# Performance work log

Hardware: AMD Instinct MI355X
Metric: run time of the kernel (lower is better)

## Reference

```python
import jax, jax.numpy as jnp
import numpy as np

D_H = 1024

def _binary_operator(e_i, e_j):
    a_i, kv_i = e_i
    a_j, kv_j = e_j
    return (a_j * a_i, a_j * kv_i + kv_j)

def setup_inputs() -> dict:
    key = jax.random.key(0)
    k1, k2 = jax.random.split(key)
    B, S, D = 4, 4096, 1024
    x = jax.random.normal(k1, (B, S, D), dtype=jnp.float32)
    # nn.Dense default lecun_normal-ish scale; plain scaled normal is fine for a reference
    W = jax.random.normal(k2, (D, 3 * D_H), dtype=jnp.float32) * (1.0 / np.sqrt(D))
    b = jnp.zeros((3 * D_H,), dtype=jnp.float32)
    return {"x": x, "W": W, "b": b}

def reference(x, W, b):
    # projection: (B,S,D) @ (D, 3*d_h)
    proj = jnp.einsum('bsd,dh->bsh', x, W) + b
    inp = jnp.tanh(proj[:, :, :D_H])                 # (B,S,d_h)
    gates = jax.nn.sigmoid(proj[:, :, D_H:])         # (B,S,2*d_h)
    input_gate, output_gate = jnp.split(gates, 2, axis=-1)
    forget_gate = 1.0 - input_gate                   # tied gates
    _, hidden = jax.lax.associative_scan(
        _binary_operator, (forget_gate, inp * input_gate), axis=1)
    return jnp.tanh(hidden) * output_gate            # (B,S,d_h)
```

## Files before the change

### kernel.cpp

```cpp
#include <hip/hip_runtime.h>
#include <hip/hip_bf16.h>
#include <cmath>

typedef _Float16 half8 __attribute__((ext_vector_type(8)));
typedef _Float16 half4 __attribute__((ext_vector_type(4)));
typedef float f32x4 __attribute__((ext_vector_type(4)));

#define M_DIM 16384
#define K_DIM 1024
#define N_DIM 3072
#define S_LEN 4096
#define NCHUNK 64
#define CLEN 64

#define OT_STRIDE 136

__device__ __forceinline__ float fast_sigmoid(float x) {
    return __builtin_amdgcn_rcpf(1.0f + __expf(-x));
}
__device__ __forceinline__ float fast_tanh(float x) {
    float t = __expf(-2.0f * __builtin_fabsf(x));
    float y = (1.0f - t) * __builtin_amdgcn_rcpf(1.0f + t);
    return __builtin_copysignf(y, x);
}

__global__ void k_cast_x(const float* __restrict__ x, _Float16* __restrict__ xb) {
    int i = blockIdx.x * blockDim.x + threadIdx.x;
    float4 v = reinterpret_cast<const float4*>(x)[i];
    half4 h;
    h.x = (_Float16)v.x; h.y = (_Float16)v.y;
    h.z = (_Float16)v.z; h.w = (_Float16)v.w;
    reinterpret_cast<half4*>(xb)[i] = h;
}

__global__ void k_cast_w(const float* __restrict__ W, _Float16* __restrict__ Wt) {
    __shared__ float t[64][65];
    const int k0 = (blockIdx.x / 48) * 64;
    const int n0 = (blockIdx.x % 48) * 64;
    const int c  = threadIdx.x & 63;
    const int r0 = threadIdx.x >> 6;
    #pragma unroll
    for (int i = 0; i < 16; ++i) {
        int r = r0 + i * 4;
        t[r][c] = W[(size_t)(k0 + r) * N_DIM + n0 + c];
    }
    __syncthreads();
    #pragma unroll
    for (int i = 0; i < 16; ++i) {
        int r = r0 + i * 4;
        Wt[(size_t)(n0 + r) * K_DIM + k0 + c] = (_Float16)t[c][r];
    }
}

__global__ __launch_bounds__(256, 3) void k_gemm(
    const _Float16* __restrict__ A,
    const _Float16* __restrict__ Bt,
    const float* __restrict__ bias,
    _Float16* __restrict__ G)
{
    __shared__ _Float16 lds[128 * OT_STRIDE];

    const int tid  = threadIdx.x;
    const int lane = tid & 63;
    const int w    = tid >> 6;
    const int wr   = w >> 1;
    const int wc   = w & 1;

    const int bid   = blockIdx.x;
    const int wg    = (bid & 7) * 384 + (bid >> 3);
    const int tileM = (wg / 24) * 128;
    const int tileN = (wg % 24) * 128;

    const int l3   = lane >> 3;
    const int c8   = lane & 7;
    const int scol = ((c8 ^ l3) << 3);
    const _Float16* gA = A  + (size_t)(tileM + w * 32 + l3) * K_DIM + scol;
    const _Float16* gB = Bt + (size_t)(tileN + w * 32 + l3) * K_DIM + scol;
    _Float16* const sA = lds + w * 2048;
    _Float16* const sB = lds + 8192 + w * 2048;

    const int l15 = lane & 15;
    const int hi  = lane >> 4;
    const int swz = (l15 & 7) << 3;
    const int o0  = (hi * 8)      ^ swz;
    const int o1  = (32 + hi * 8) ^ swz;
    const _Float16* arow = lds + (wr * 64 + l15) * 64;
    const _Float16* brow = lds + 8192 + (wc * 64 + l15) * 64;

    f32x4 acc[4][4] = {};

#define GL(SRC, DST) __builtin_amdgcn_global_load_lds( \
        (const __attribute__((address_space(1))) void*)(SRC), \
        (__attribute__((address_space(3))) void*)(DST), 16, 0, 0)

#define STAGE(kt) do { \
        const _Float16* ga_ = gA + (size_t)(kt) * 64; \
        const _Float16* gb_ = gB + (size_t)(kt) * 64; \
        GL(ga_,                       sA);        \
        GL(ga_ + (size_t) 8 * K_DIM,  sA + 512);  \
        GL(ga_ + (size_t)16 * K_DIM,  sA + 1024); \
        GL(ga_ + (size_t)24 * K_DIM,  sA + 1536); \
        GL(gb_,                       sB);        \
        GL(gb_ + (size_t) 8 * K_DIM,  sB + 512);  \
        GL(gb_ + (size_t)16 * K_DIM,  sB + 1024); \
        GL(gb_ + (size_t)24 * K_DIM,  sB + 1536); \
    } while (0)

#define SCHED0() __builtin_amdgcn_sched_barrier(0)

    STAGE(0);
    asm volatile("s_waitcnt vmcnt(0)" ::: "memory");
    __builtin_amdgcn_s_barrier();
    asm volatile("" ::: "memory");

    #pragma unroll 1
    for (int kt = 0; kt < 16; ++kt) {
        half8 a[4][2], b[4][2];
        #pragma unroll
        for (int m = 0; m < 4; ++m) {
            a[m][0] = *(const half8*)(arow + m * 1024 + o0);
            a[m][1] = *(const half8*)(arow + m * 1024 + o1);
            b[m][0] = *(const half8*)(brow + m * 1024 + o0);
            b[m][1] = *(const half8*)(brow + m * 1024 + o1);
        }
        asm volatile("s_waitcnt lgkmcnt(0)" ::: "memory");
        SCHED0();
        __builtin_amdgcn_s_barrier();

        if (kt < 15) STAGE(kt + 1);
        SCHED0();

        __builtin_amdgcn_s_setprio(1);
        #pragma unroll
        for (int m = 0; m < 4; ++m)
            #pragma unroll
            for (int n = 0; n < 4; ++n)
                acc[m][n] = __builtin_amdgcn_mfma_f32_16x16x32_f16(
                    a[m][0], b[n][0], acc[m][n], 0, 0, 0);
        #pragma unroll
        for (int m = 0; m < 4; ++m)
            #pragma unroll
            for (int n = 0; n < 4; ++n)
                acc[m][n] = __builtin_amdgcn_mfma_f32_16x16x32_f16(
                    a[m][1], b[n][1], acc[m][n], 0, 0, 0);
        __builtin_amdgcn_s_setprio(0);
        SCHED0();

        if (kt < 15) {
            asm volatile("s_waitcnt vmcnt(0)" ::: "memory");
            __builtin_amdgcn_s_barrier();
            asm volatile("" ::: "memory");
        }
    }
#undef STAGE
#undef GL

    #pragma unroll
    for (int j = 0; j < 4; ++j) {
        const int n  = wc * 64 + j * 16 + l15;
        const int gn = tileN + n;
        const float bn = bias[gn];
        const bool is_tanh = (gn < 1024);
        #pragma unroll
        for (int i = 0; i < 4; ++i) {
            const int rb = wr * 64 + i * 16 + hi * 4;
            #pragma unroll
            for (int r = 0; r < 4; ++r) {
                float v = acc[i][j][r] + bn;
                lds[(rb + r) * OT_STRIDE + n] =
                    (_Float16)(is_tanh ? fast_tanh(v) : fast_sigmoid(v));
            }
        }
    }
    __syncthreads();
    {
        const int row = tid >> 4;
        const int col = (tid & 15) * 8;
        #pragma unroll
        for (int itr = 0; itr < 8; ++itr) {
            const int rr = row + itr * 16;
            half8 vv = *(const half8*)(lds + rr * OT_STRIDE + col);
            *(half8*)(G + (size_t)(tileM + rr) * N_DIM + tileN + col) = vv;
        }
    }
}

__global__ void k_scan1(const _Float16* __restrict__ G,
                        float* __restrict__ sumA, float* __restrict__ sumH) {
    const int chunk = blockIdx.x & 63;
    const int b     = blockIdx.x >> 6;
    const int d0    = threadIdx.x * 4;

    const _Float16* base = G + (size_t)(b * S_LEN + chunk * CLEN) * N_DIM;
    float A[4], H[4];
    #pragma unroll
    for (int j = 0; j < 4; ++j) { A[j] = 1.0f; H[j] = 0.0f; }
    #pragma unroll 4
    for (int s = 0; s < CLEN; ++s) {
        half4 v0 = *(const half4*)(base + (size_t)s * N_DIM + d0);
        half4 v1 = *(const half4*)(base + (size_t)s * N_DIM + 1024 + d0);
        #pragma unroll
        for (int j = 0; j < 4; ++j) {
            float g1 = (float)v1[j];
            float a  = 1.0f - g1;
            H[j] = fmaf(a, H[j], (float)v0[j] * g1);
            A[j] *= a;
        }
    }
    const int cidx = (b * NCHUNK + chunk) * 1024 + d0;
    *(float4*)(sumA + cidx) = make_float4(A[0], A[1], A[2], A[3]);
    *(float4*)(sumH + cidx) = make_float4(H[0], H[1], H[2], H[3]);
}

__global__ void k_scan2(const float* __restrict__ sumA, const float* __restrict__ sumH,
                        float* __restrict__ pref) {
    const int c = blockIdx.x * blockDim.x + threadIdx.x;
    const int b = c >> 10;
    const int d = c & 1023;
    float h = 0.0f;
    #pragma unroll 8
    for (int chunk = 0; chunk < NCHUNK; ++chunk) {
        const int idx = (b * NCHUNK + chunk) * 1024 + d;
        pref[idx] = h;
        h = fmaf(sumA[idx], h, sumH[idx]);
    }
}

__global__ void k_scan3(const _Float16* __restrict__ G,
                        const float* __restrict__ pref,
                        float* __restrict__ out) {
    const int chunk = blockIdx.x & 63;
    const int b     = blockIdx.x >> 6;
    const int d0    = threadIdx.x * 4;

    const _Float16* base = G + (size_t)(b * S_LEN + chunk * CLEN) * N_DIM;
    const int cidx = (b * NCHUNK + chunk) * 1024 + d0;
    float h[4];
    #pragma unroll
    for (int j = 0; j < 4; ++j) h[j] = pref[cidx + j];

    #pragma unroll 2
    for (int s = 0; s < CLEN; ++s) {
        half4 v0 = *(const half4*)(base + (size_t)s * N_DIM + d0);
        half4 v1 = *(const half4*)(base + (size_t)s * N_DIM + 1024 + d0);
        half4 v2 = *(const half4*)(base + (size_t)s * N_DIM + 2048 + d0);
        float4 o;
        #pragma unroll
        for (int j = 0; j < 4; ++j) {
            float g1 = (float)v1[j];
            float a  = 1.0f - g1;
            h[j] = fmaf(a, h[j], (float)v0[j] * g1);
            ((float*)&o)[j] = fast_tanh(h[j]) * (float)v2[j];
        }
        *(float4*)(out + (size_t)(b * S_LEN + chunk * CLEN + s) * 1024 + d0) = o;
    }
}

extern "C" void kernel_launch(void* const* d_in, const int* in_sizes, int n_in,
                              void* d_out, int out_size, void* d_ws, size_t ws_size,
                              hipStream_t stream) {
    const float* x = (const float*)d_in[0];
    const float* W = (const float*)d_in[1];
    const float* b = (const float*)d_in[2];
    float* out = (float*)d_out;

    char* ws = (char*)d_ws;
    _Float16* xb = (_Float16*)ws;
    _Float16* Wt = (_Float16*)(ws + 33554432);
    _Float16* G  = (_Float16*)(ws + 33554432 + 6291456);
    float* sumA  = (float*)(ws + 140509184);
    float* sumH  = sumA + 4096 * NCHUNK;
    float* pref  = sumH + 4096 * NCHUNK;

    k_cast_x<<<16384, 256, 0, stream>>>(x, xb);
    k_cast_w<<<768,   256, 0, stream>>>(W, Wt);
    k_gemm <<<3072, 256, 0, stream>>>(xb, Wt, b, G);
    k_scan1<<<256, 256, 0, stream>>>(G, sumA, sumH);
    k_scan2<<<16,  256, 0, stream>>>(sumA, sumH, pref);
    k_scan3<<<256, 256, 0, stream>>>(G, pref, out);
    (void)in_sizes; (void)n_in; (void)out_size; (void)ws_size;
}
```

Baseline: 192.5 us.

## Merge cast kernels and move gate activations from GEMM epilogue into scans

Combines the x and W fp16 cast kernels into one launch with a block-index split. The GEMM epilogue now writes raw biased pre-activations, and tanh/sigmoid are applied inside the scan kernels instead. The aim is a shorter GEMM epilogue, with the activations overlapping the memory-bound scan loads, and one fewer launch. In exchange, scan1 and scan3 both recompute the input and forget activations, and pre-activations rather than activations are now rounded to fp16. scan3's unroll is also raised from 2 to 4.

```diff
diff --git a/kernel.cpp b/kernel.cpp
--- a/kernel.cpp
+++ b/kernel.cpp
@@ -24,31 +24,33 @@
     return __builtin_copysignf(y, x);
 }
 
-__global__ void k_cast_x(const float* __restrict__ x, _Float16* __restrict__ xb) {
-    int i = blockIdx.x * blockDim.x + threadIdx.x;
-    float4 v = reinterpret_cast<const float4*>(x)[i];
-    half4 h;
-    h.x = (_Float16)v.x; h.y = (_Float16)v.y;
-    h.z = (_Float16)v.z; h.w = (_Float16)v.w;
-    reinterpret_cast<half4*>(xb)[i] = h;
-}
-
-__global__ void k_cast_w(const float* __restrict__ W, _Float16* __restrict__ Wt) {
+__global__ void k_cast(const float* __restrict__ x, _Float16* __restrict__ xb,
+                       const float* __restrict__ W, _Float16* __restrict__ Wt) {
     __shared__ float t[64][65];
-    const int k0 = (blockIdx.x / 48) * 64;
-    const int n0 = (blockIdx.x % 48) * 64;
-    const int c  = threadIdx.x & 63;
-    const int r0 = threadIdx.x >> 6;
-    #pragma unroll
-    for (int i = 0; i < 16; ++i) {
-        int r = r0 + i * 4;
-        t[r][c] = W[(size_t)(k0 + r) * N_DIM + n0 + c];
-    }
-    __syncthreads();
-    #pragma unroll
-    for (int i = 0; i < 16; ++i) {
-        int r = r0 + i * 4;
-        Wt[(size_t)(n0 + r) * K_DIM + k0 + c] = (_Float16)t[c][r];
+    if (blockIdx.x < 16384) {
+        int i = blockIdx.x * blockDim.x + threadIdx.x;
+        float4 v = reinterpret_cast<const float4*>(x)[i];
+        half4 h;
+        h.x = (_Float16)v.x; h.y = (_Float16)v.y;
+        h.z = (_Float16)v.z; h.w = (_Float16)v.w;
+        reinterpret_cast<half4*>(xb)[i] = h;
+    } else {
+        const int wb = blockIdx.x - 16384;
+        const int k0 = (wb / 48) * 64;
+        const int n0 = (wb % 48) * 64;
+        const int c  = threadIdx.x & 63;
+        const int r0 = threadIdx.x >> 6;
+        #pragma unroll
+        for (int i = 0; i < 16; ++i) {
+            int r = r0 + i * 4;
+            t[r][c] = W[(size_t)(k0 + r) * N_DIM + n0 + c];
+        }
+        __syncthreads();
+        #pragma unroll
+        for (int i = 0; i < 16; ++i) {
+            int r = r0 + i * 4;
+            Wt[(size_t)(n0 + r) * K_DIM + k0 + c] = (_Float16)t[c][r];
+        }
     }
 }
 
@@ -158,18 +160,13 @@
     #pragma unroll
     for (int j = 0; j < 4; ++j) {
         const int n  = wc * 64 + j * 16 + l15;
-        const int gn = tileN + n;
-        const float bn = bias[gn];
-        const bool is_tanh = (gn < 1024);
+        const float bn = bias[tileN + n];
         #pragma unroll
         for (int i = 0; i < 4; ++i) {
             const int rb = wr * 64 + i * 16 + hi * 4;
             #pragma unroll
-            for (int r = 0; r < 4; ++r) {
-                float v = acc[i][j][r] + bn;
-                lds[(rb + r) * OT_STRIDE + n] =
-                    (_Float16)(is_tanh ? fast_tanh(v) : fast_sigmoid(v));
-            }
+            for (int r = 0; r < 4; ++r)
+                lds[(rb + r) * OT_STRIDE + n] = (_Float16)(acc[i][j][r] + bn);
         }
     }
     __syncthreads();
@@ -201,9 +198,10 @@
         half4 v1 = *(const half4*)(base + (size_t)s * N_DIM + 1024 + d0);
         #pragma unroll
         for (int j = 0; j < 4; ++j) {
-            float g1 = (float)v1[j];
+            float g0 = fast_tanh((float)v0[j]);
+            float g1 = fast_sigmoid((float)v1[j]);
             float a  = 1.0f - g1;
-            H[j] = fmaf(a, H[j], (float)v0[j] * g1);
+            H[j] = fmaf(a, H[j], g0 * g1);
             A[j] *= a;
         }
     }
@@ -239,7 +237,7 @@
     #pragma unroll
     for (int j = 0; j < 4; ++j) h[j] = pref[cidx + j];
 
-    #pragma unroll 2
+    #pragma unroll 4
     for (int s = 0; s < CLEN; ++s) {
         half4 v0 = *(const half4*)(base + (size_t)s * N_DIM + d0);
         half4 v1 = *(const half4*)(base + (size_t)s * N_DIM + 1024 + d0);
@@ -247,10 +245,12 @@
         float4 o;
         #pragma unroll
         for (int j = 0; j < 4; ++j) {
-            float g1 = (float)v1[j];
+            float g0 = fast_tanh((float)v0[j]);
+            float g1 = fast_sigmoid((float)v1[j]);
+            float g2 = fast_sigmoid((float)v2[j]);
             float a  = 1.0f - g1;
-            h[j] = fmaf(a, h[j], (float)v0[j] * g1);
-            ((float*)&o)[j] = fast_tanh(h[j]) * (float)v2[j];
+            h[j] = fmaf(a, h[j], g0 * g1);
+            ((float*)&o)[j] = fast_tanh(h[j]) * g2;
         }
         *(float4*)(out + (size_t)(b * S_LEN + chunk * CLEN + s) * 1024 + d0) = o;
     }
@@ -272,8 +272,7 @@
     float* sumH  = sumA + 4096 * NCHUNK;
     float* pref  = sumH + 4096 * NCHUNK;
 
-    k_cast_x<<<16384, 256, 0, stream>>>(x, xb);
-    k_cast_w<<<768,   256, 0, stream>>>(W, Wt);
+    k_cast <<<17152, 256, 0, stream>>>(x, xb, W, Wt);
     k_gemm <<<3072, 256, 0, stream>>>(xb, Wt, b, G);
     k_scan1<<<256, 256, 0, stream>>>(G, sumA, sumH);
     k_scan2<<<16,  256, 0, stream>>>(sumA, sumH, pref);
```

Result: no change. 194.1 us (+0.8%).
